# Optimization experiments

Hardware: AMD Instinct MI355X
Metric: run time of the kernel (lower is better)

Reference implementation:

```python
import jax, jax.numpy as jnp
import numpy as np

TOP_K = 2
ROUTING_SCALE = 1.0
SCORE_FUNC = 'softmax'  # matches init_kwargs


def setup_inputs() -> dict:
    key = jax.random.key(0)
    k1, k2 = jax.random.split(key)
    x = jax.random.normal(k1, (16384, 2048), dtype=jnp.float32)
    # router weight: nn.Linear(hidden, experts).weight has shape [experts, hidden], init std=0.02
    W = jax.random.normal(k2, (64, 2048), dtype=jnp.float32) * 0.02
    return {"x": x, "W": W}


def reference(x, W):
    # scores = x @ W.T : [tokens, num_experts]
    scores = jnp.einsum('th,eh->te', x, W)
    # original_scores is detached in the torch code
    original_scores = jax.lax.stop_gradient(scores)
    if SCORE_FUNC == 'softmax':
        probs = jax.nn.softmax(scores, axis=-1)
    else:
        probs = jax.nn.sigmoid(scores)
    # top-k over experts (torch uses sorted=False; selected set/values identical)
    _, top_k_indices = jax.lax.top_k(probs, TOP_K)
    routing_weights = jnp.take_along_axis(original_scores, top_k_indices, axis=-1)
    if SCORE_FUNC == 'sigmoid':
        routing_weights = routing_weights / (routing_weights.sum(axis=-1, keepdims=True) + 1e-06)
    routing_weights = routing_weights * ROUTING_SCALE
    return routing_weights, top_k_indices
```

## Files before the change

kernel.cpp:

```cpp
#include <hip/hip_runtime.h>
#include <stdint.h>

#define KDIM 2048
#define NEXP 64
#define MT   64
#define KC   32
#define NTHR 512
#define NTOK 16384

typedef _Float16 half8 __attribute__((ext_vector_type(8)));
typedef __fp16  fp16x2 __attribute__((ext_vector_type(2)));
typedef float f32x4 __attribute__((ext_vector_type(4)));

__device__ __forceinline__ int swz(int row, int byte_in_row) {
    return ((row << 6) + byte_in_row) ^ ((row & 14) << 3);
}

__device__ __forceinline__ uint32_t pkrtz(float a, float b) {
    fp16x2 h = __builtin_amdgcn_cvt_pkrtz(a, b);
    return __builtin_bit_cast(uint32_t, h);
}

__device__ __forceinline__ void split4(float4 v, uint2* hv, uint2* lv) {
    float y[4] = {v.x, v.y, v.z, v.w};
    uint32_t hw[2], lw[2];
    #pragma unroll
    for (int i = 0; i < 2; ++i) {
        float y0 = y[2 * i], y1 = y[2 * i + 1];
        float h0 = __builtin_bit_cast(float, __builtin_bit_cast(uint32_t, y0) & 0xFFFFE000u);
        float h1 = __builtin_bit_cast(float, __builtin_bit_cast(uint32_t, y1) & 0xFFFFE000u);
        hw[i] = pkrtz(h0, h1);
        lw[i] = pkrtz(y0 - h0, y1 - h1);
    }
    hv->x = hw[0]; hv->y = hw[1];
    lv->x = lw[0]; lv->y = lw[1];
}

#define VMCNT4() do { asm volatile("s_waitcnt vmcnt(4)" ::: "memory"); \
                      __builtin_amdgcn_sched_barrier(0); } while (0)
#define VMCNT0() do { asm volatile("s_waitcnt vmcnt(0)" ::: "memory"); \
                      __builtin_amdgcn_sched_barrier(0); } while (0)
#define LGKM_BAR() do { asm volatile("s_waitcnt lgkmcnt(0)" ::: "memory"); \
                        __builtin_amdgcn_sched_barrier(0);                 \
                        __builtin_amdgcn_s_barrier();                      \
                        __builtin_amdgcn_sched_barrier(0); } while (0)

__global__ __launch_bounds__(NTHR) void router_kernel(const float* __restrict__ x,
                                                      const float* __restrict__ W,
                                                      float* __restrict__ out_w,
                                                      float* __restrict__ out_i) {
    __shared__ char AsB[2][2][2][4096];
    __shared__ char BsB[2][2][2][4096];

    const int tid  = threadIdx.x;
    const int lane = tid & 63;
    const int wave = tid >> 6;
    const int g    = wave >> 2;
    const int wm   = (wave >> 1) & 1;
    const int wn   = wave & 1;
    const int tidg = tid & 255;
    const int tb   = blockIdx.x * MT;
    const int kb0  = g * (KDIM / 2);

    const int xrow0 = tidg >> 3;
    const int xseg  = tidg & 7;
    const float* xsrc0 = x + (size_t)(tb + xrow0) * KDIM + kb0 + xseg * 4;
    const float* xsrc1 = x + (size_t)(tb + xrow0 + 32) * KDIM + kb0 + xseg * 4;
    const int xoff0 = swz(xrow0, xseg * 8);
    const int xoff1 = swz(xrow0 + 32, xseg * 8);
    const int wrr = tidg >> 2;
    const int wss = tidg & 3;
    const float* wsrc = W + (size_t)wrr * KDIM + kb0 + wss * 8;
    const int woff = swz(wrr, wss * 16);

    const int kb = lane >> 4;
    const int ra0 = wm * 32 + (lane & 15);
    const int rb0 = wn * 32 + (lane & 15);
    const int aoff0 = swz(ra0,      kb * 16);
    const int aoff1 = swz(ra0 + 16, kb * 16);
    const int boff0 = swz(rb0,      kb * 16);
    const int boff1 = swz(rb0 + 16, kb * 16);

    f32x4 acc[2][2];
    #pragma unroll
    for (int i = 0; i < 2; ++i)
        #pragma unroll
        for (int j = 0; j < 2; ++j)
            acc[i][j] = (f32x4){0.f, 0.f, 0.f, 0.f};

    float4 Ax0, Ax1, Aw0, Aw1;
    float4 Bx0, Bx1, Bw0, Bw1;

#define LOADM(X0, X1, W0, W1, c)                                           \
    do {                                                                   \
        X0 = *reinterpret_cast<const float4*>(xsrc0 + (c) * KC);           \
        X1 = *reinterpret_cast<const float4*>(xsrc1 + (c) * KC);           \
        W0 = *reinterpret_cast<const float4*>(wsrc + (c) * KC);            \
        W1 = *reinterpret_cast<const float4*>(wsrc + (c) * KC + 4);        \
    } while (0)

    auto STORE = [&](int b, float4 v0, float4 v1, float4 w0, float4 w1) {
        uint2 hv, lv;
        split4(v0, &hv, &lv);
        *reinterpret_cast<uint2*>(&AsB[g][b][0][0] + xoff0) = hv;
        *reinterpret_cast<uint2*>(&AsB[g][b][1][0] + xoff0) = lv;
        split4(v1, &hv, &lv);
        *reinterpret_cast<uint2*>(&AsB[g][b][0][0] + xoff1) = hv;
        *reinterpret_cast<uint2*>(&AsB[g][b][1][0] + xoff1) = lv;
        uint2 h0, l0, h1, l1;
        split4(w0, &h0, &l0);
        split4(w1, &h1, &l1);
        uint4 wh = {h0.x, h0.y, h1.x, h1.y};
        uint4 wl = {l0.x, l0.y, l1.x, l1.y};
        *reinterpret_cast<uint4*>(&BsB[g][b][0][0] + woff) = wh;
        *reinterpret_cast<uint4*>(&BsB[g][b][1][0] + woff) = wl;
    };

    auto COMPUTE = [&](int b) {
        half8 ah[2], al[2], bh[2], bl[2];
        ah[0] = *reinterpret_cast<const half8*>(&AsB[g][b][0][0] + aoff0);
        ah[1] = *reinterpret_cast<const half8*>(&AsB[g][b][0][0] + aoff1);
        al[0] = *reinterpret_cast<const half8*>(&AsB[g][b][1][0] + aoff0);
        al[1] = *reinterpret_cast<const half8*>(&AsB[g][b][1][0] + aoff1);
        bh[0] = *reinterpret_cast<const half8*>(&BsB[g][b][0][0] + boff0);
        bh[1] = *reinterpret_cast<const half8*>(&BsB[g][b][0][0] + boff1);
        bl[0] = *reinterpret_cast<const half8*>(&BsB[g][b][1][0] + boff0);
        bl[1] = *reinterpret_cast<const half8*>(&BsB[g][b][1][0] + boff1);
        #pragma unroll
        for (int m = 0; m < 2; ++m)
            #pragma unroll
            for (int n = 0; n < 2; ++n) {
                acc[m][n] = __builtin_amdgcn_mfma_f32_16x16x32_f16(ah[m], bh[n], acc[m][n], 0, 0, 0);
                acc[m][n] = __builtin_amdgcn_mfma_f32_16x16x32_f16(al[m], bh[n], acc[m][n], 0, 0, 0);
                acc[m][n] = __builtin_amdgcn_mfma_f32_16x16x32_f16(ah[m], bl[n], acc[m][n], 0, 0, 0);
            }
    };

    LOADM(Ax0, Ax1, Aw0, Aw1, 0);
    LOADM(Bx0, Bx1, Bw0, Bw1, 1);
    VMCNT4();
    STORE(0, Ax0, Ax1, Aw0, Aw1);
    LGKM_BAR();

    for (int q = 0; q < 15; ++q) {
        COMPUTE(0);
        LOADM(Ax0, Ax1, Aw0, Aw1, 2 * q + 2);
        VMCNT4();
        STORE(1, Bx0, Bx1, Bw0, Bw1);
        LGKM_BAR();
        COMPUTE(1);
        LOADM(Bx0, Bx1, Bw0, Bw1, 2 * q + 3);
        VMCNT4();
        STORE(0, Ax0, Ax1, Aw0, Aw1);
        LGKM_BAR();
    }
    COMPUTE(0);
    VMCNT0();
    STORE(1, Bx0, Bx1, Bw0, Bw1);
    LGKM_BAR();
    COMPUTE(1);

    __syncthreads();
    float (*ss)[NEXP + 3] = reinterpret_cast<float (*)[NEXP + 3]>(&AsB[0][0][0][0]);
    if (g == 0) {
        #pragma unroll
        for (int m = 0; m < 2; ++m)
            #pragma unroll
            for (int n = 0; n < 2; ++n)
                #pragma unroll
                for (int r = 0; r < 4; ++r) {
                    int tok = wm * 32 + m * 16 + (lane >> 4) * 4 + r;
                    int e   = wn * 32 + n * 16 + (lane & 15);
                    ss[tok][e] = acc[m][n][r];
                }
    }
    __syncthreads();
    if (g == 1) {
        #pragma unroll
        for (int m = 0; m < 2; ++m)
            #pragma unroll
            for (int n = 0; n < 2; ++n)
                #pragma unroll
                for (int r = 0; r < 4; ++r) {
                    int tok = wm * 32 + m * 16 + (lane >> 4) * 4 + r;
                    int e   = wn * 32 + n * 16 + (lane & 15);
                    ss[tok][e] += acc[m][n][r];
                }
    }
    __syncthreads();

    if (tid < MT) {
        const int t = tid;
        float m1 = -1e30f, m2 = -1e30f;
        int i1 = 0, i2 = 0;
        #pragma unroll
        for (int e = 0; e < NEXP; ++e) {
            float v = ss[t][e];
            if (v > m1) { m2 = m1; i2 = i1; m1 = v; i1 = e; }
            else if (v > m2) { m2 = v; i2 = e; }
        }
        const int gt = tb + t;
        out_w[gt * 2 + 0] = m1;
        out_w[gt * 2 + 1] = m2;
        out_i[gt * 2 + 0] = (float)i1;
        out_i[gt * 2 + 1] = (float)i2;
    }
#undef LOADM
}

extern "C" void kernel_launch(void* const* d_in, const int* in_sizes, int n_in,
                              void* d_out, int out_size, void* d_ws, size_t ws_size,
                              hipStream_t stream) {
    const float* x = (const float*)d_in[0];
    const float* W = (const float*)d_in[1];
    float* out = (float*)d_out;

    const int n_tokens = in_sizes[0] / KDIM;

    hipLaunchKernelGGL(router_kernel, dim3(n_tokens / MT), dim3(NTHR), 0, stream,
                       x, W, out, out + 2 * (size_t)n_tokens);
}
```

Before: 31.27 us.

## Split K across four wave groups per block with 1024 threads

```diff
diff --git a/kernel.cpp b/kernel.cpp
--- a/kernel.cpp
+++ b/kernel.cpp
@@ -5,7 +5,8 @@
 #define NEXP 64
 #define MT   64
 #define KC   32
-#define NTHR 512
+#define NG   4
+#define NTHR 1024
 #define NTOK 16384
 
 typedef _Float16 half8 __attribute__((ext_vector_type(8)));
@@ -49,8 +50,7 @@
                                                       const float* __restrict__ W,
                                                       float* __restrict__ out_w,
                                                       float* __restrict__ out_i) {
-    __shared__ char AsB[2][2][2][4096];
-    __shared__ char BsB[2][2][2][4096];
+    __shared__ char SM[NG * 32768];
 
     const int tid  = threadIdx.x;
     const int lane = tid & 63;
@@ -60,7 +60,10 @@
     const int wn   = wave & 1;
     const int tidg = tid & 255;
     const int tb   = blockIdx.x * MT;
-    const int kb0  = g * (KDIM / 2);
+    const int kb0  = g * (KDIM / NG);
+
+    char* Ab = SM + g * 32768;
+    char* Bb = Ab + 16384;
 
     const int xrow0 = tidg >> 3;
     const int xseg  = tidg & 7;
@@ -102,30 +105,30 @@
     auto STORE = [&](int b, float4 v0, float4 v1, float4 w0, float4 w1) {
         uint2 hv, lv;
         split4(v0, &hv, &lv);
-        *reinterpret_cast<uint2*>(&AsB[g][b][0][0] + xoff0) = hv;
-        *reinterpret_cast<uint2*>(&AsB[g][b][1][0] + xoff0) = lv;
+        *reinterpret_cast<uint2*>(Ab + b * 8192        + xoff0) = hv;
+        *reinterpret_cast<uint2*>(Ab + b * 8192 + 4096 + xoff0) = lv;
         split4(v1, &hv, &lv);
-        *reinterpret_cast<uint2*>(&AsB[g][b][0][0] + xoff1) = hv;
-        *reinterpret_cast<uint2*>(&AsB[g][b][1][0] + xoff1) = lv;
+        *reinterpret_cast<uint2*>(Ab + b * 8192        + xoff1) = hv;
+        *reinterpret_cast<uint2*>(Ab + b * 8192 + 4096 + xoff1) = lv;
         uint2 h0, l0, h1, l1;
         split4(w0, &h0, &l0);
         split4(w1, &h1, &l1);
         uint4 wh = {h0.x, h0.y, h1.x, h1.y};
         uint4 wl = {l0.x, l0.y, l1.x, l1.y};
-        *reinterpret_cast<uint4*>(&BsB[g][b][0][0] + woff) = wh;
-        *reinterpret_cast<uint4*>(&BsB[g][b][1][0] + woff) = wl;
+        *reinterpret_cast<uint4*>(Bb + b * 8192        + woff) = wh;
+        *reinterpret_cast<uint4*>(Bb + b * 8192 + 4096 + woff) = wl;
     };
 
     auto COMPUTE = [&](int b) {
         half8 ah[2], al[2], bh[2], bl[2];
-        ah[0] = *reinterpret_cast<const half8*>(&AsB[g][b][0][0] + aoff0);
-        ah[1] = *reinterpret_cast<const half8*>(&AsB[g][b][0][0] + aoff1);
-        al[0] = *reinterpret_cast<const half8*>(&AsB[g][b][1][0] + aoff0);
-        al[1] = *reinterpret_cast<const half8*>(&AsB[g][b][1][0] + aoff1);
-        bh[0] = *reinterpret_cast<const half8*>(&BsB[g][b][0][0] + boff0);
-        bh[1] = *reinterpret_cast<const half8*>(&BsB[g][b][0][0] + boff1);
-        bl[0] = *reinterpret_cast<const half8*>(&BsB[g][b][1][0] + boff0);
-        bl[1] = *reinterpret_cast<const half8*>(&BsB[g][b][1][0] + boff1);
+        ah[0] = *reinterpret_cast<const half8*>(Ab + b * 8192        + aoff0);
+        ah[1] = *reinterpret_cast<const half8*>(Ab + b * 8192        + aoff1);
+        al[0] = *reinterpret_cast<const half8*>(Ab + b * 8192 + 4096 + aoff0);
+        al[1] = *reinterpret_cast<const half8*>(Ab + b * 8192 + 4096 + aoff1);
+        bh[0] = *reinterpret_cast<const half8*>(Bb + b * 8192        + boff0);
+        bh[1] = *reinterpret_cast<const half8*>(Bb + b * 8192        + boff1);
+        bl[0] = *reinterpret_cast<const half8*>(Bb + b * 8192 + 4096 + boff0);
+        bl[1] = *reinterpret_cast<const half8*>(Bb + b * 8192 + 4096 + boff1);
         #pragma unroll
         for (int m = 0; m < 2; ++m)
             #pragma unroll
@@ -142,7 +145,7 @@
     STORE(0, Ax0, Ax1, Aw0, Aw1);
     LGKM_BAR();
 
-    for (int q = 0; q < 15; ++q) {
+    for (int q = 0; q < 7; ++q) {
         COMPUTE(0);
         LOADM(Ax0, Ax1, Aw0, Aw1, 2 * q + 2);
         VMCNT4();
@@ -161,41 +164,30 @@
     COMPUTE(1);
 
     __syncthreads();
-    float (*ss)[NEXP + 3] = reinterpret_cast<float (*)[NEXP + 3]>(&AsB[0][0][0][0]);
-    if (g == 0) {
-        #pragma unroll
-        for (int m = 0; m < 2; ++m)
+    float (*ssg)[NEXP + 3] = reinterpret_cast<float (*)[NEXP + 3]>(SM + g * 17408);
+    #pragma unroll
+    for (int m = 0; m < 2; ++m)
+        #pragma unroll
+        for (int n = 0; n < 2; ++n)
             #pragma unroll
-            for (int n = 0; n < 2; ++n)
-                #pragma unroll
-                for (int r = 0; r < 4; ++r) {
-                    int tok = wm * 32 + m * 16 + (lane >> 4) * 4 + r;
-                    int e   = wn * 32 + n * 16 + (lane & 15);
-                    ss[tok][e] = acc[m][n][r];
-                }
-    }
-    __syncthreads();
-    if (g == 1) {
-        #pragma unroll
-        for (int m = 0; m < 2; ++m)
-            #pragma unroll
-            for (int n = 0; n < 2; ++n)
-                #pragma unroll
-                for (int r = 0; r < 4; ++r) {
-                    int tok = wm * 32 + m * 16 + (lane >> 4) * 4 + r;
-                    int e   = wn * 32 + n * 16 + (lane & 15);
-                    ss[tok][e] += acc[m][n][r];
-                }
-    }
+            for (int r = 0; r < 4; ++r) {
+                int tok = wm * 32 + m * 16 + (lane >> 4) * 4 + r;
+                int e   = wn * 32 + n * 16 + (lane & 15);
+                ssg[tok][e] = acc[m][n][r];
+            }
     __syncthreads();
 
     if (tid < MT) {
         const int t = tid;
+        const float (*s0)[NEXP + 3] = reinterpret_cast<const float (*)[NEXP + 3]>(SM);
+        const float (*s1)[NEXP + 3] = reinterpret_cast<const float (*)[NEXP + 3]>(SM + 17408);
+        const float (*s2)[NEXP + 3] = reinterpret_cast<const float (*)[NEXP + 3]>(SM + 2 * 17408);
+        const float (*s3)[NEXP + 3] = reinterpret_cast<const float (*)[NEXP + 3]>(SM + 3 * 17408);
         float m1 = -1e30f, m2 = -1e30f;
         int i1 = 0, i2 = 0;
         #pragma unroll
         for (int e = 0; e < NEXP; ++e) {
-            float v = ss[t][e];
+            float v = (s0[t][e] + s1[t][e]) + (s2[t][e] + s3[t][e]);
             if (v > m1) { m2 = m1; i2 = i1; m1 = v; i1 = e; }
             else if (v > m2) { m2 = v; i2 = e; }
         }
```

New measurement: 32.53 us. +4.0%, slower.
